# Optimization experiments

Hardware: AMD Instinct MI355X
Metric: run time of the kernel (lower is better)

## Reference

```python
import jax, jax.numpy as jnp
import numpy as np

# Each of the 16 soft binary logic ops is a polynomial c0 + c1*a + c2*b + c3*a*b.
# Rows below are the [c0, c1, c2, c3] coefficients for ops 0..15 (same math as bin_op).
_OP_COEF = np.array([
    [0., 0., 0., 0.],   # 0: zeros
    [0., 0., 0., 1.],   # 1: a*b
    [0., 1., 0., -1.],  # 2: a - a*b
    [0., 1., 0., 0.],   # 3: a
    [0., 0., 1., -1.],  # 4: b - a*b
    [0., 0., 1., 0.],   # 5: b
    [0., 1., 1., -2.],  # 6: a + b - 2ab
    [0., 1., 1., -1.],  # 7: a + b - ab
    [1., -1., -1., 1.], # 8: 1 - (a + b - ab)
    [1., -1., -1., 2.], # 9: 1 - (a + b - 2ab)
    [1., 0., -1., 0.],  # 10: 1 - b
    [1., 0., -1., 1.],  # 11: 1 - b + ab
    [1., -1., 0., 0.],  # 12: 1 - a
    [1., -1., 0., 1.],  # 13: 1 - a + ab
    [1., 0., 0., -1.],  # 14: 1 - a*b
    [1., 0., 0., 0.],   # 15: ones
], dtype=np.float32)

K_CLASSES = 10
TAU = 30.0


def logic_layer(x, w, idx_a, idx_b):
    # x: [B, in_dim], w: [out_dim, 16], idx_a/idx_b: [out_dim]
    probs = jax.nn.softmax(w, axis=-1)                 # [O, 16]
    coef = probs @ jnp.asarray(_OP_COEF)               # [O, 4]
    a = x[:, idx_a]                                    # [B, O]
    b = x[:, idx_b]                                    # [B, O]
    # weighted mixture of 16 ops == polynomial in (1, a, b, a*b)
    return coef[:, 0] + coef[:, 1] * a + coef[:, 2] * b + coef[:, 3] * (a * b)


def group_sum(x, k, tau):
    B = x.shape[0]
    return x.reshape(B, k, x.shape[-1] // k).sum(-1) / tau


def setup_inputs() -> dict:
    key = jax.random.key(0)
    ks = jax.random.split(key, 10)
    B, D0, D1, D2, D3 = 4096, 1024, 8192, 8192, 10240
    return {
        "x": jax.random.uniform(ks[0], (B, D0), dtype=jnp.float32),
        "w1": jax.random.normal(ks[1], (D1, 16), dtype=jnp.float32),
        "w2": jax.random.normal(ks[2], (D2, 16), dtype=jnp.float32),
        "w3": jax.random.normal(ks[3], (D3, 16), dtype=jnp.float32),
        "idx_a1": jax.random.randint(ks[4], (D1,), 0, D0, dtype=jnp.int32),
        "idx_b1": jax.random.randint(ks[5], (D1,), 0, D0, dtype=jnp.int32),
        "idx_a2": jax.random.randint(ks[6], (D2,), 0, D1, dtype=jnp.int32),
        "idx_b2": jax.random.randint(ks[7], (D2,), 0, D1, dtype=jnp.int32),
        "idx_a3": jax.random.randint(ks[8], (D3,), 0, D2, dtype=jnp.int32),
        "idx_b3": jax.random.randint(ks[9], (D3,), 0, D2, dtype=jnp.int32),
    }


def reference(x, w1, w2, w3, idx_a1, idx_b1, idx_a2, idx_b2, idx_a3, idx_b3):
    h = logic_layer(x, w1, idx_a1, idx_b1)
    h = logic_layer(h, w2, idx_a2, idx_b2)
    h = logic_layer(h, w3, idx_a3, idx_b3)
    return group_sum(h, K_CLASSES, TAU)   # [B, 10]
```

## Files before the change

### kernel.cpp

```cpp
#include <hip/hip_runtime.h>
#include <hip/hip_fp16.h>
#include <stdint.h>

#define D0 1024
#define D1 8192
#define D2 8192
#define D3 10240
#define B_ROWS 4096

#define SM_XB     0
#define SM_H2     16384
#define SM_CSUM   (16384 + 131072)
#define SM_BYTES  (16384 + 131072 + 320)

__device__ __forceinline__ float4 softmax_coef(const float* __restrict__ w) {
    const float4* wv = (const float4*)w;
    float4 q0 = wv[0], q1 = wv[1], q2 = wv[2], q3 = wv[3];
    float wa[16] = {q0.x, q0.y, q0.z, q0.w, q1.x, q1.y, q1.z, q1.w,
                    q2.x, q2.y, q2.z, q2.w, q3.x, q3.y, q3.z, q3.w};
    float m = wa[0];
#pragma unroll
    for (int i = 1; i < 16; ++i) m = fmaxf(m, wa[i]);
    float e[16], s = 0.f;
#pragma unroll
    for (int i = 0; i < 16; ++i) { e[i] = __expf(wa[i] - m); s += e[i]; }
    float inv = 1.f / s;
    static constexpr float OPC[16][4] = {
        {0.f, 0.f, 0.f, 0.f}, {0.f, 0.f, 0.f, 1.f}, {0.f, 1.f, 0.f, -1.f}, {0.f, 1.f, 0.f, 0.f},
        {0.f, 0.f, 1.f, -1.f}, {0.f, 0.f, 1.f, 0.f}, {0.f, 1.f, 1.f, -2.f}, {0.f, 1.f, 1.f, -1.f},
        {1.f, -1.f, -1.f, 1.f}, {1.f, -1.f, -1.f, 2.f}, {1.f, 0.f, -1.f, 0.f}, {1.f, 0.f, -1.f, 1.f},
        {1.f, -1.f, 0.f, 0.f}, {1.f, -1.f, 0.f, 1.f}, {1.f, 0.f, 0.f, -1.f}, {1.f, 0.f, 0.f, 0.f}};
    float c0 = 0.f, c1 = 0.f, c2 = 0.f, c3 = 0.f;
#pragma unroll
    for (int i = 0; i < 16; ++i) {
        float p = e[i] * inv;
        c0 += p * OPC[i][0];
        c1 += p * OPC[i][1];
        c2 += p * OPC[i][2];
        c3 += p * OPC[i][3];
    }
    return make_float4(c0, c1, c2, c3);
}

__device__ __forceinline__ uint2 pack_coef(float4 c) {
    uint2 r;
    r.x = __builtin_bit_cast(uint32_t, __floats2half2_rn(c.x, c.y));
    r.y = __builtin_bit_cast(uint32_t, __floats2half2_rn(c.z, c.w));
    return r;
}

#define PREP_TOTAL (3 * D2 + D3)
__global__ __launch_bounds__(256) void prep_kernel(
    const float* __restrict__ w1, const float* __restrict__ w2,
    const float* __restrict__ w3,
    const int* __restrict__ ia1, const int* __restrict__ ib1,
    const int* __restrict__ ia2, const int* __restrict__ ib2,
    const int* __restrict__ ia3, const int* __restrict__ ib3,
    uint4* __restrict__ bcM1, uint4* __restrict__ bcM2,
    uint4* __restrict__ d3M) {
    int G = blockIdx.x * 256 + threadIdx.x;
    if (G < D2) {
        int g = G;
        int pa = ia2[g], pb = ib2[g];
        float4 cO = softmax_coef(w2 + (size_t)g * 16);
        uint32_t xiA = (uint32_t)(ia1[pa] << 4) | ((uint32_t)(ib1[pa] << 4) << 16);
        uint32_t xiB = (uint32_t)(ia1[pb] << 4) | ((uint32_t)(ib1[pb] << 4) << 16);
        uint2 o = pack_coef(cO);
        bcM1[g] = make_uint4(xiA, xiB, o.x, o.y);
    } else if (G < 2 * D2) {
        int g = G - D2;
        int pa = ia2[g];
        uint2 a = pack_coef(softmax_coef(w1 + (size_t)pa * 16));
        ((uint2*)bcM2)[2 * g] = a;
    } else if (G < 3 * D2) {
        int g = G - 2 * D2;
        int pb = ib2[g];
        uint2 b = pack_coef(softmax_coef(w1 + (size_t)pb * 16));
        ((uint2*)bcM2)[2 * g + 1] = b;
    } else {
        int g = G - 3 * D2;
        float4 cO = softmax_coef(w3 + (size_t)g * 16);
        uint2 o = pack_coef(cO);
        uint32_t ei = (uint32_t)ia3[g] | ((uint32_t)ib3[g] << 16);
        d3M[g] = make_uint4(ei, o.x, o.y, 0u);
    }
}

__device__ __forceinline__ uint4 gate8(uint4 av, uint4 bv, uint2 cf) {
    __half2 p = __builtin_bit_cast(__half2, cf.x);
    __half2 q = __builtin_bit_cast(__half2, cf.y);
    __half2 c0 = __low2half2(p), c1 = __high2half2(p);
    __half2 c2 = __low2half2(q), c3 = __high2half2(q);
    uint4 r;
#pragma unroll
    for (int i = 0; i < 4; ++i) {
        __half2 a = __builtin_bit_cast(__half2, (&av.x)[i]);
        __half2 b = __builtin_bit_cast(__half2, (&bv.x)[i]);
        __half2 h = __hfma2(a, __hfma2(b, c3, c1), __hfma2(b, c2, c0));
        (&r.x)[i] = __builtin_bit_cast(uint32_t, h);
    }
    return r;
}

__device__ __forceinline__ float dpp_sum_f32(float x) {
#define DPPADD(ctrl, rmask)                                              \
    x += __builtin_bit_cast(float, __builtin_amdgcn_update_dpp(          \
             0, __builtin_bit_cast(int, x), (ctrl), (rmask), 0xf, true))
    DPPADD(0x111, 0xf);
    DPPADD(0x112, 0xf);
    DPPADD(0x114, 0xf);
    DPPADD(0x118, 0xf);
    DPPADD(0x142, 0xa);
    DPPADD(0x143, 0xc);
#undef DPPADD
    return x;
}

__global__ __launch_bounds__(1024, 4) void fused_kernel(
    const float* __restrict__ x, const uint4* __restrict__ bcM1,
    const uint4* __restrict__ bcM2, const uint4* __restrict__ d3M,
    float* __restrict__ out) {
    extern __shared__ char sm[];
    uint4* xb = (uint4*)(sm + SM_XB);
    float* csum = (float*)(sm + SM_CSUM);

    const int t = threadIdx.x;
    const int rowbase = blockIdx.x << 3;
    const int tg = t << 1;

    uint4 m1a_n = bcM1[tg];
    uint4 m1b_n = bcM1[tg + 1];

    {
        const float* xp = x + (size_t)rowbase * D0 + t;
        uint4 v;
#pragma unroll
        for (int i = 0; i < 4; ++i) {
            float va = xp[(size_t)(2 * i) * D0];
            float vb = xp[(size_t)(2 * i + 1) * D0];
            (&v.x)[i] = __builtin_bit_cast(uint32_t, __floats2half2_rn(va, vb));
        }
        xb[t] = v;
    }
    if (t < 80) csum[t] = 0.f;
    __syncthreads();

#pragma unroll
    for (int k = 0; k < 4; ++k) {
        uint4 m1a = m1a_n, m1b = m1b_n;
        int g = tg + (k << 11);
        uint4 m2a = bcM2[g];
        uint4 m2b = bcM2[g + 1];
        if (k < 3) {
            int gn = tg + ((k + 1) << 11);
            m1a_n = bcM1[gn];
            m1b_n = bcM1[gn + 1];
        }
        uint4 aa0 = *(const uint4*)(sm + (m1a.x & 0xffffu));
        uint4 ab0 = *(const uint4*)(sm + (m1a.x >> 16));
        uint4 ba0 = *(const uint4*)(sm + (m1a.y & 0xffffu));
        uint4 bb0 = *(const uint4*)(sm + (m1a.y >> 16));
        uint4 aa1 = *(const uint4*)(sm + (m1b.x & 0xffffu));
        uint4 ab1 = *(const uint4*)(sm + (m1b.x >> 16));
        uint4 ba1 = *(const uint4*)(sm + (m1b.y & 0xffffu));
        uint4 bb1 = *(const uint4*)(sm + (m1b.y >> 16));
        uint4 h0 = gate8(gate8(aa0, ab0, make_uint2(m2a.x, m2a.y)),
                         gate8(ba0, bb0, make_uint2(m2a.z, m2a.w)),
                         make_uint2(m1a.z, m1a.w));
        uint4 h1v = gate8(gate8(aa1, ab1, make_uint2(m2b.x, m2b.y)),
                          gate8(ba1, bb1, make_uint2(m2b.z, m2b.w)),
                          make_uint2(m1b.z, m1b.w));
        *(uint4*)(sm + SM_H2 + ((uint32_t)g << 4)) = h0;
        *(uint4*)(sm + SM_H2 + ((uint32_t)(g + 1) << 4)) = h1v;
    }
    __syncthreads();

    {
        const int wv = t >> 6, lane = t & 63;
        const int gbase = wv * 640;
        const int cA = gbase >> 10;
        const int bnd = (cA + 1) << 10;
        const bool cross = (gbase + 640 > bnd);
        float s0[8] = {0.f, 0.f, 0.f, 0.f, 0.f, 0.f, 0.f, 0.f};
        float s1[8] = {0.f, 0.f, 0.f, 0.f, 0.f, 0.f, 0.f, 0.f};
#pragma unroll
        for (int j = 0; j < 5; ++j) {
            int gc = gbase + (j << 7);
            int g = gc + (lane << 1);
            uint4 ma = d3M[g];
            uint4 mb = d3M[g + 1];
            uint4 av0 = *(const uint4*)(sm + SM_H2 + ((ma.x & 0xffffu) << 4));
            uint4 bv0 = *(const uint4*)(sm + SM_H2 + ((ma.x >> 16) << 4));
            uint4 av1 = *(const uint4*)(sm + SM_H2 + ((mb.x & 0xffffu) << 4));
            uint4 bv1 = *(const uint4*)(sm + SM_H2 + ((mb.x >> 16) << 4));
            uint4 h0 = gate8(av0, bv0, make_uint2(ma.y, ma.z));
            uint4 h1v = gate8(av1, bv1, make_uint2(mb.y, mb.z));
            float pr8[8];
#pragma unroll
            for (int i = 0; i < 4; ++i) {
                __half2 pr = __hadd2(__builtin_bit_cast(__half2, (&h0.x)[i]),
                                     __builtin_bit_cast(__half2, (&h1v.x)[i]));
                pr8[2 * i] = __low2float(pr);
                pr8[2 * i + 1] = __high2float(pr);
            }
            if (gc < bnd) {
#pragma unroll
                for (int r = 0; r < 8; ++r) s0[r] += pr8[r];
            } else {
#pragma unroll
                for (int r = 0; r < 8; ++r) s1[r] += pr8[r];
            }
        }
#pragma unroll
        for (int r = 0; r < 8; ++r) s0[r] = dpp_sum_f32(s0[r]);
        if (cross) {
#pragma unroll
            for (int r = 0; r < 8; ++r) s1[r] = dpp_sum_f32(s1[r]);
        }
        if (lane == 63) {
#pragma unroll
            for (int r = 0; r < 8; ++r) atomicAdd(&csum[cA * 8 + r], s0[r]);
            if (cross) {
#pragma unroll
                for (int r = 0; r < 8; ++r) atomicAdd(&csum[(cA + 1) * 8 + r], s1[r]);
            }
        }
    }
    __syncthreads();

    if (t < 80) {
        int c = t >> 3, r = t & 7;
        out[(size_t)(rowbase + r) * 10 + c] = csum[t] * (1.0f / 30.0f);
    }
}

extern "C" void kernel_launch(void* const* d_in, const int* in_sizes, int n_in,
                              void* d_out, int out_size, void* d_ws, size_t ws_size,
                              hipStream_t stream) {
    const float* x = (const float*)d_in[0];
    const float* w1 = (const float*)d_in[1];
    const float* w2 = (const float*)d_in[2];
    const float* w3 = (const float*)d_in[3];
    const int* ia1 = (const int*)d_in[4];
    const int* ib1 = (const int*)d_in[5];
    const int* ia2 = (const int*)d_in[6];
    const int* ib2 = (const int*)d_in[7];
    const int* ia3 = (const int*)d_in[8];
    const int* ib3 = (const int*)d_in[9];
    float* out = (float*)d_out;

    char* p = (char*)d_ws;
    uint4* bcM1 = (uint4*)p;    p += (size_t)D2 * 16;
    uint4* bcM2 = (uint4*)p;    p += (size_t)D2 * 16;
    uint4* d3M = (uint4*)p;

    hipFuncSetAttribute(reinterpret_cast<const void*>(fused_kernel),
                        hipFuncAttributeMaxDynamicSharedMemorySize, SM_BYTES);

    prep_kernel<<<PREP_TOTAL / 256, 256, 0, stream>>>(
        w1, w2, w3, ia1, ib1, ia2, ib2, ia3, ib3, bcM1, bcM2, d3M);
    fused_kernel<<<B_ROWS / 8, 1024, SM_BYTES, stream>>>(x, bcM1, bcM2, d3M, out);
}
```

Baseline: 99.78 us.

## Process two 8-row tiles per block, prefetching second tile's input into registers

Each block now handles 16 batch rows in two sequential passes of 8, and the grid is halved. The second tile's x values are loaded into registers at the start, so their global latency overlaps the first pass's compute. Per-thread metadata indexing changes from paired (2t, 2t+1) to strided (t, t+1024), which makes the global loads more coalesced. The trade-off is fewer blocks in flight, which may reduce latency hiding across the GPU and leaves the two passes in a block running serially.

```diff
diff --git a/kernel.cpp b/kernel.cpp
--- a/kernel.cpp
+++ b/kernel.cpp
@@ -116,45 +116,20 @@
     return x;
 }
 
-__global__ __launch_bounds__(1024, 4) void fused_kernel(
-    const float* __restrict__ x, const uint4* __restrict__ bcM1,
-    const uint4* __restrict__ bcM2, const uint4* __restrict__ d3M,
-    float* __restrict__ out) {
-    extern __shared__ char sm[];
-    uint4* xb = (uint4*)(sm + SM_XB);
-    float* csum = (float*)(sm + SM_CSUM);
-
-    const int t = threadIdx.x;
-    const int rowbase = blockIdx.x << 3;
-    const int tg = t << 1;
-
-    uint4 m1a_n = bcM1[tg];
-    uint4 m1b_n = bcM1[tg + 1];
-
-    {
-        const float* xp = x + (size_t)rowbase * D0 + t;
-        uint4 v;
-#pragma unroll
-        for (int i = 0; i < 4; ++i) {
-            float va = xp[(size_t)(2 * i) * D0];
-            float vb = xp[(size_t)(2 * i + 1) * D0];
-            (&v.x)[i] = __builtin_bit_cast(uint32_t, __floats2half2_rn(va, vb));
-        }
-        xb[t] = v;
-    }
-    if (t < 80) csum[t] = 0.f;
-    __syncthreads();
-
+__device__ __forceinline__ void stage_bc(char* sm, int t,
+                                         const uint4* __restrict__ bcM1,
+                                         const uint4* __restrict__ bcM2,
+                                         uint4 m1a_n, uint4 m1b_n) {
 #pragma unroll
     for (int k = 0; k < 4; ++k) {
         uint4 m1a = m1a_n, m1b = m1b_n;
-        int g = tg + (k << 11);
-        uint4 m2a = bcM2[g];
-        uint4 m2b = bcM2[g + 1];
+        int g0 = t + (k << 11);
+        int g1 = g0 + 1024;
+        uint4 m2a = bcM2[g0];
+        uint4 m2b = bcM2[g1];
         if (k < 3) {
-            int gn = tg + ((k + 1) << 11);
-            m1a_n = bcM1[gn];
-            m1b_n = bcM1[gn + 1];
+            m1a_n = bcM1[g0 + 2048];
+            m1b_n = bcM1[g1 + 2048];
         }
         uint4 aa0 = *(const uint4*)(sm + (m1a.x & 0xffffu));
         uint4 ab0 = *(const uint4*)(sm + (m1a.x >> 16));
@@ -170,67 +145,127 @@
         uint4 h1v = gate8(gate8(aa1, ab1, make_uint2(m2b.x, m2b.y)),
                           gate8(ba1, bb1, make_uint2(m2b.z, m2b.w)),
                           make_uint2(m1b.z, m1b.w));
-        *(uint4*)(sm + SM_H2 + ((uint32_t)g << 4)) = h0;
-        *(uint4*)(sm + SM_H2 + ((uint32_t)(g + 1) << 4)) = h1v;
-    }
-    __syncthreads();
-
+        *(uint4*)(sm + SM_H2 + ((uint32_t)g0 << 4)) = h0;
+        *(uint4*)(sm + SM_H2 + ((uint32_t)g1 << 4)) = h1v;
+    }
+}
+
+__device__ __forceinline__ void stage_d(char* sm, int t,
+                                        const uint4* __restrict__ d3M,
+                                        float* csum) {
+    const int wv = t >> 6, lane = t & 63;
+    const int gbase = wv * 640;
+    const int cA = gbase >> 10;
+    const int bnd = (cA + 1) << 10;
+    const bool cross = (gbase + 640 > bnd);
+    float s0[8] = {0.f, 0.f, 0.f, 0.f, 0.f, 0.f, 0.f, 0.f};
+    float s1[8] = {0.f, 0.f, 0.f, 0.f, 0.f, 0.f, 0.f, 0.f};
+#pragma unroll
+    for (int j = 0; j < 5; ++j) {
+        int gc = gbase + (j << 7);
+        uint4 ma = d3M[gc + lane];
+        uint4 mb = d3M[gc + 64 + lane];
+        uint4 av0 = *(const uint4*)(sm + SM_H2 + ((ma.x & 0xffffu) << 4));
+        uint4 bv0 = *(const uint4*)(sm + SM_H2 + ((ma.x >> 16) << 4));
+        uint4 av1 = *(const uint4*)(sm + SM_H2 + ((mb.x & 0xffffu) << 4));
+        uint4 bv1 = *(const uint4*)(sm + SM_H2 + ((mb.x >> 16) << 4));
+        uint4 h0 = gate8(av0, bv0, make_uint2(ma.y, ma.z));
+        uint4 h1v = gate8(av1, bv1, make_uint2(mb.y, mb.z));
+        float pr8[8];
+#pragma unroll
+        for (int i = 0; i < 4; ++i) {
+            __half2 pr = __hadd2(__builtin_bit_cast(__half2, (&h0.x)[i]),
+                                 __builtin_bit_cast(__half2, (&h1v.x)[i]));
+            pr8[2 * i] = __low2float(pr);
+            pr8[2 * i + 1] = __high2float(pr);
+        }
+        if (gc < bnd) {
+#pragma unroll
+            for (int r = 0; r < 8; ++r) s0[r] += pr8[r];
+        } else {
+#pragma unroll
+            for (int r = 0; r < 8; ++r) s1[r] += pr8[r];
+        }
+    }
+#pragma unroll
+    for (int r = 0; r < 8; ++r) s0[r] = dpp_sum_f32(s0[r]);
+    if (cross) {
+#pragma unroll
+        for (int r = 0; r < 8; ++r) s1[r] = dpp_sum_f32(s1[r]);
+    }
+    if (lane == 63) {
+#pragma unroll
+        for (int r = 0; r < 8; ++r) atomicAdd(&csum[cA * 8 + r], s0[r]);
+        if (cross) {
+#pragma unroll
+            for (int r = 0; r < 8; ++r) atomicAdd(&csum[(cA + 1) * 8 + r], s1[r]);
+        }
+    }
+}
+
+__global__ __launch_bounds__(1024, 4) void fused_kernel(
+    const float* __restrict__ x, const uint4* __restrict__ bcM1,
+    const uint4* __restrict__ bcM2, const uint4* __restrict__ d3M,
+    float* __restrict__ out) {
+    extern __shared__ char sm[];
+    uint4* xb = (uint4*)(sm + SM_XB);
+    float* csum = (float*)(sm + SM_CSUM);
+
+    const int t = threadIdx.x;
+    const int rowbase = blockIdx.x << 4;
+
+    uint4 m1a_n = bcM1[t];
+    uint4 m1b_n = bcM1[t + 1024];
+
+    const float* xp = x + (size_t)rowbase * D0 + t;
+    float x2r[8];
+#pragma unroll
+    for (int i = 0; i < 8; ++i) x2r[i] = xp[(size_t)(8 + i) * D0];
     {
-        const int wv = t >> 6, lane = t & 63;
-        const int gbase = wv * 640;
-        const int cA = gbase >> 10;
-        const int bnd = (cA + 1) << 10;
-        const bool cross = (gbase + 640 > bnd);
-        float s0[8] = {0.f, 0.f, 0.f, 0.f, 0.f, 0.f, 0.f, 0.f};
-        float s1[8] = {0.f, 0.f, 0.f, 0.f, 0.f, 0.f, 0.f, 0.f};
-#pragma unroll
-        for (int j = 0; j < 5; ++j) {
-            int gc = gbase + (j << 7);
-            int g = gc + (lane << 1);
-            uint4 ma = d3M[g];
-            uint4 mb = d3M[g + 1];
-            uint4 av0 = *(const uint4*)(sm + SM_H2 + ((ma.x & 0xffffu) << 4));
-            uint4 bv0 = *(const uint4*)(sm + SM_H2 + ((ma.x >> 16) << 4));
-            uint4 av1 = *(const uint4*)(sm + SM_H2 + ((mb.x & 0xffffu) << 4));
-            uint4 bv1 = *(const uint4*)(sm + SM_H2 + ((mb.x >> 16) << 4));
-            uint4 h0 = gate8(av0, bv0, make_uint2(ma.y, ma.z));
-            uint4 h1v = gate8(av1, bv1, make_uint2(mb.y, mb.z));
-            float pr8[8];
-#pragma unroll
-            for (int i = 0; i < 4; ++i) {
-                __half2 pr = __hadd2(__builtin_bit_cast(__half2, (&h0.x)[i]),
-                                     __builtin_bit_cast(__half2, (&h1v.x)[i]));
-                pr8[2 * i] = __low2float(pr);
-                pr8[2 * i + 1] = __high2float(pr);
-            }
-            if (gc < bnd) {
-#pragma unroll
-                for (int r = 0; r < 8; ++r) s0[r] += pr8[r];
-            } else {
-#pragma unroll
-                for (int r = 0; r < 8; ++r) s1[r] += pr8[r];
-            }
-        }
-#pragma unroll
-        for (int r = 0; r < 8; ++r) s0[r] = dpp_sum_f32(s0[r]);
-        if (cross) {
-#pragma unroll
-            for (int r = 0; r < 8; ++r) s1[r] = dpp_sum_f32(s1[r]);
-        }
-        if (lane == 63) {
-#pragma unroll
-            for (int r = 0; r < 8; ++r) atomicAdd(&csum[cA * 8 + r], s0[r]);
-            if (cross) {
-#pragma unroll
-                for (int r = 0; r < 8; ++r) atomicAdd(&csum[(cA + 1) * 8 + r], s1[r]);
-            }
-        }
-    }
+        uint4 v;
+#pragma unroll
+        for (int i = 0; i < 4; ++i) {
+            float va = xp[(size_t)(2 * i) * D0];
+            float vb = xp[(size_t)(2 * i + 1) * D0];
+            (&v.x)[i] = __builtin_bit_cast(uint32_t, __floats2half2_rn(va, vb));
+        }
+        xb[t] = v;
+    }
+    if (t < 80) csum[t] = 0.f;
+    __syncthreads();
+
+    stage_bc(sm, t, bcM1, bcM2, m1a_n, m1b_n);
+    __syncthreads();
+
+    {
+        uint4 v;
+#pragma unroll
+        for (int i = 0; i < 4; ++i)
+            (&v.x)[i] = __builtin_bit_cast(
+                uint32_t, __floats2half2_rn(x2r[2 * i], x2r[2 * i + 1]));
+        xb[t] = v;
+    }
+    m1a_n = bcM1[t];
+    m1b_n = bcM1[t + 1024];
+
+    stage_d(sm, t, d3M, csum);
     __syncthreads();
 
     if (t < 80) {
         int c = t >> 3, r = t & 7;
         out[(size_t)(rowbase + r) * 10 + c] = csum[t] * (1.0f / 30.0f);
+        csum[t] = 0.f;
+    }
+
+    stage_bc(sm, t, bcM1, bcM2, m1a_n, m1b_n);
+    __syncthreads();
+
+    stage_d(sm, t, d3M, csum);
+    __syncthreads();
+
+    if (t < 80) {
+        int c = t >> 3, r = t & 7;
+        out[(size_t)(rowbase + 8 + r) * 10 + c] = csum[t] * (1.0f / 30.0f);
     }
 }
 
@@ -259,5 +294,5 @@
 
     prep_kernel<<<PREP_TOTAL / 256, 256, 0, stream>>>(
         w1, w2, w3, ia1, ib1, ia2, ib2, ia3, ib3, bcM1, bcM2, d3M);
-    fused_kernel<<<B_ROWS / 8, 1024, SM_BYTES, stream>>>(x, bcM1, bcM2, d3M, out);
-}
+    fused_kernel<<<B_ROWS / 16, 1024, SM_BYTES, stream>>>(x, bcM1, bcM2, d3M, out);
+}
```

After: 98.92 us. Within noise of the previous version (-0.9%).
